# Kernel tuning notes

Measured on AMD Instinct MI355X. Metric: run time of the kernel, lower is better.

Reference implementation:

```python
import jax, jax.numpy as jnp
import numpy as np

D_MODEL = 1024
N_HEADS = 16
D_HEAD = D_MODEL // N_HEADS


def setup_inputs() -> dict:
    key = jax.random.key(0)
    ks = jax.random.split(key, 11)
    B, S = 2, 2048
    scale = 1.0 / np.sqrt(D_MODEL)
    inp = {
        "query": jax.random.normal(ks[0], (B, S, D_MODEL), jnp.float32),
        "key": jax.random.normal(ks[1], (B, S, D_MODEL), jnp.float32),
        "value": jax.random.normal(ks[2], (B, S, D_MODEL), jnp.float32),
        "Wq": jax.random.normal(ks[3], (D_MODEL, D_MODEL), jnp.float32) * scale,
        "bq": jnp.zeros((D_MODEL,), jnp.float32),
        "Wk": jax.random.normal(ks[4], (D_MODEL, D_MODEL), jnp.float32) * scale,
        "bk": jnp.zeros((D_MODEL,), jnp.float32),
        "Wv": jax.random.normal(ks[5], (D_MODEL, D_MODEL), jnp.float32) * scale,
        "bv": jnp.zeros((D_MODEL,), jnp.float32),
        "Wo": jax.random.normal(ks[6], (D_MODEL, D_MODEL), jnp.float32) * scale,
        "bo": jnp.zeros((D_MODEL,), jnp.float32),
    }
    return inp


def _split_heads(x):
    B, S, _ = x.shape
    return x.reshape(B, S, N_HEADS, D_HEAD).transpose(0, 2, 1, 3)  # [B,H,S,Dh]


def reference(query, key, value, Wq, bq, Wk, bk, Wv, bv, Wo, bo):
    q = _split_heads(query @ Wq + bq)
    k = _split_heads(key @ Wk + bk)
    v = _split_heads(value @ Wv + bv)
    # scores [B,H,S,S] -- faithfully materialized as in the original
    scores = jnp.einsum("bhqd,bhkd->bhqk", q, k) / np.sqrt(D_HEAD)
    attn = jax.nn.softmax(scores, axis=-1)
    out = jnp.einsum("bhqk,bhkd->bhqd", attn, v)  # [B,H,S,Dh]
    B, H, S, Dh = out.shape
    out = out.transpose(0, 2, 1, 3).reshape(B, S, H * Dh)
    return out @ Wo + bo
```

## Files before the change

kernel.cpp:

```cpp
#include <hip/hip_runtime.h>
#include <hip/hip_bf16.h>

using bf16 = __hip_bfloat16;
typedef __bf16 bf16x8 __attribute__((ext_vector_type(8)));
typedef __bf16 bf16x2v __attribute__((ext_vector_type(2)));
typedef float f32x4 __attribute__((ext_vector_type(4)));

#define SEQ 2048
#define DM  1024
#define QSCALE 0.18033688011112042f

__device__ __forceinline__ f32x4 mfma16(bf16x8 a, bf16x8 b, f32x4 c) {
  return __builtin_amdgcn_mfma_f32_16x16x32_bf16(a, b, c, 0, 0, 0);
}
__device__ __forceinline__ void gload16(const void* g, void* l) {
  __builtin_amdgcn_global_load_lds(
      (const __attribute__((address_space(1))) unsigned int*)g,
      (__attribute__((address_space(3))) unsigned int*)l, 16, 0, 0);
}
__device__ __forceinline__ unsigned short bfbits(float x) {
  bf16 h = __float2bfloat16(x);
  return *reinterpret_cast<unsigned short*>(&h);
}
__device__ __forceinline__ unsigned pk2(float a, float b) {
#if __has_builtin(__builtin_amdgcn_cvt_pk_bf16_f32)
  bf16x2v r = __builtin_amdgcn_cvt_pk_bf16_f32(a, b);
  return *reinterpret_cast<unsigned*>(&r);
#else
  return (unsigned)bfbits(a) | ((unsigned)bfbits(b) << 16);
#endif
}
__device__ __forceinline__ float fexp2(float x) {
#if __has_builtin(__builtin_amdgcn_exp2f)
  return __builtin_amdgcn_exp2f(x);
#else
  return exp2f(x);
#endif
}

__global__ __launch_bounds__(256) void cast_x(const float* __restrict__ q,
                                              const float* __restrict__ k,
                                              const float* __restrict__ v,
                                              bf16* __restrict__ Lx) {
  const float* src = blockIdx.y == 0 ? q : (blockIdx.y == 1 ? k : v);
  bf16* dst = Lx + (size_t)blockIdx.y * (4096ull * 1024) + (size_t)blockIdx.x * 16384;
#pragma unroll
  for (int i = 0; i < 8; ++i) {
    int u = threadIdx.x + i * 256;
    int k32 = u >> 6, l = u & 63;
    const float* p = src + (size_t)(blockIdx.x * 16 + (l & 15)) * 1024 + k32 * 32 + (l >> 4) * 8;
    float4 a = *(const float4*)p;
    float4 b = *(const float4*)(p + 4);
    alignas(16) unsigned o[4] = {pk2(a.x, a.y), pk2(a.z, a.w), pk2(b.x, b.y), pk2(b.z, b.w)};
    *(uint4*)(dst + (size_t)u * 8) = *(const uint4*)o;
  }
}

__global__ __launch_bounds__(256) void cast_w(const float* __restrict__ Wq,
                                              const float* __restrict__ Wk,
                                              const float* __restrict__ Wv,
                                              const float* __restrict__ Wo,
                                              bf16* __restrict__ Lw,
                                              bf16* __restrict__ Lwo) {
  const int widx = blockIdx.z;
  const float* W = widx == 0 ? Wq : (widx == 1 ? Wk : (widx == 2 ? Wv : Wo));
  bf16* dst = widx < 3 ? (Lw + (size_t)widx * 1048576) : Lwo;
  __shared__ float tf[64][68];
  const int t = threadIdx.x, bx = blockIdx.x, by = blockIdx.y;
#pragma unroll
  for (int i = 0; i < 4; ++i) {
    int u = t + i * 256, r = u >> 4, c4 = u & 15;
    *(float4*)&tf[r][c4 * 4] = *(const float4*)(W + (size_t)(by * 64 + r) * 1024 + bx * 64 + c4 * 4);
  }
  __syncthreads();
#pragma unroll
  for (int i = 0; i < 2; ++i) {
    int u = t + i * 256;
    int sub = u >> 6, l = u & 63;
    int n16l = sub >> 1, k32l = sub & 1;
    int nn = n16l * 16 + (l & 15);
    int kk = k32l * 32 + (l >> 4) * 8;
    alignas(16) unsigned o[4];
#pragma unroll
    for (int p = 0; p < 4; ++p) o[p] = pk2(tf[kk + 2 * p][nn], tf[kk + 2 * p + 1][nn]);
    size_t off = ((((size_t)(bx * 4 + n16l)) * 32 + (by * 2 + k32l)) * 64 + l) * 8;
    *(uint4*)(dst + off) = *(const uint4*)o;
  }
}

__global__ __launch_bounds__(256) void qkv_gemm(const bf16* __restrict__ Lw,
                                                const bf16* __restrict__ Lx,
                                                const float* __restrict__ bq,
                                                const float* __restrict__ bk,
                                                const float* __restrict__ bv,
                                                bf16* __restrict__ Lq,
                                                bf16* __restrict__ Lk,
                                                bf16* __restrict__ Lv) {
  __shared__ alignas(16) bf16 Wl[8192];
  __shared__ alignas(16) bf16 Xl[8192];
  const int t = threadIdx.x, lane = t & 63, w = t >> 6;
  const int m16 = lane & 15, g4 = lane >> 4;
  const int third = blockIdx.y >> 3, mtl = blockIdx.y & 7, nt = blockIdx.x;
  const int wm = w >> 1, wn = w & 1;
  const bf16* Wb = Lw + (size_t)third * 1048576;
  const bf16* Xb = Lx + (size_t)third * (4096ull * 1024);
  f32x4 acc[4][4] = {};

  for (int slab = 0; slab < 16; ++slab) {
#pragma unroll
    for (int ii = 0; ii < 4; ++ii) {
      int s = w * 4 + ii;
      const bf16* gp = Wb + ((((size_t)(mtl * 8 + (s >> 1))) * 32 + slab * 2 + (s & 1)) * 64 + lane) * 8;
      gload16(gp, (void*)&Wl[s * 512]);
    }
#pragma unroll
    for (int ii = 0; ii < 4; ++ii) {
      int s = w * 4 + ii;
      const bf16* gp = Xb + ((((size_t)(nt * 8 + (s >> 1))) * 32 + slab * 2 + (s & 1)) * 64 + lane) * 8;
      gload16(gp, (void*)&Xl[s * 512]);
    }
    __syncthreads();
#pragma unroll
    for (int c = 0; c < 2; ++c) {
      bf16x8 wf[4], xf[4];
#pragma unroll
      for (int i = 0; i < 4; ++i) wf[i] = *(const bf16x8*)&Wl[((wm * 4 + i) * 2 + c) * 512 + lane * 8];
#pragma unroll
      for (int j = 0; j < 4; ++j) xf[j] = *(const bf16x8*)&Xl[((wn * 4 + j) * 2 + c) * 512 + lane * 8];
      if (third < 2) {
#pragma unroll
        for (int i = 0; i < 4; ++i)
#pragma unroll
          for (int j = 0; j < 4; ++j) acc[i][j] = mfma16(wf[i], xf[j], acc[i][j]);
      } else {
#pragma unroll
        for (int i = 0; i < 4; ++i)
#pragma unroll
          for (int j = 0; j < 4; ++j) acc[i][j] = mfma16(xf[i], wf[j], acc[i][j]);
      }
    }
    __syncthreads();
  }

  if (third < 2) {
    bf16* dst = third == 0 ? Lq : Lk;
    const float* bias = third == 0 ? bq : bk;
    const float sc = third == 0 ? QSCALE : 1.0f;
#pragma unroll
    for (int i = 0; i < 4; ++i) {
      int doutb = mtl * 128 + wm * 64 + i * 16 + g4 * 4;
      float4 b4 = *(const float4*)(bias + doutb);
      int hh = doutb >> 6, d32 = (doutb & 63) >> 5;
      int lhi = (doutb & 31) >> 3, half = g4 & 1;
#pragma unroll
      for (int j = 0; j < 4; ++j) {
        int seq = nt * 128 + wn * 64 + j * 16 + m16;
        int bb = seq >> 11, s16w = (seq & 2047) >> 4;
        size_t off = ((((size_t)(bb * 128 + s16w)) * 16 + hh) * 2 + d32) * 512 + (m16 + 16 * lhi) * 8 + half * 4;
        uint2 pv;
        pv.x = pk2((acc[i][j][0] + b4.x) * sc, (acc[i][j][1] + b4.y) * sc);
        pv.y = pk2((acc[i][j][2] + b4.z) * sc, (acc[i][j][3] + b4.w) * sc);
        *(uint2*)(dst + off) = pv;
      }
    }
  } else {
#pragma unroll
    for (int j = 0; j < 4; ++j) {
      int dout = mtl * 128 + wm * 64 + j * 16 + m16;
      float bvv = bv[dout];
      int hh = dout >> 6, dt = (dout & 63) >> 4;
#pragma unroll
      for (int i = 0; i < 4; ++i) {
        int seqb = nt * 128 + wn * 64 + i * 16 + g4 * 4;
        int bb = seqb >> 11, kt = (seqb & 2047) >> 6, ks32 = (seqb & 63) >> 5;
        int lhi = (seqb & 31) >> 3, half = g4 & 1;
        size_t off = (((((size_t)(bb * 32 + kt)) * 16 + hh) * 4 + dt) * 2 + ks32) * 512 + (m16 + 16 * lhi) * 8 + half * 4;
        uint2 pv;
        pv.x = pk2(acc[i][j][0] + bvv, acc[i][j][1] + bvv);
        pv.y = pk2(acc[i][j][2] + bvv, acc[i][j][3] + bvv);
        *(uint2*)(Lv + off) = pv;
      }
    }
  }
}

__global__ __launch_bounds__(256) void flash(const bf16* __restrict__ Lq,
                                             const bf16* __restrict__ Lk,
                                             const bf16* __restrict__ Lv,
                                             bf16* __restrict__ Lab) {
  __shared__ alignas(16) bf16 Kl[2][4096];
  __shared__ alignas(16) bf16 Vl[2][4096];
  __shared__ alignas(16) bf16 Pt[4][32][68];
  const int t = threadIdx.x, lane = t & 63, w = t >> 6;
  const int m16 = lane & 15, g4 = lane >> 4;
  const int bid = blockIdx.x;
  const int qt = bid & 15, h = (bid >> 4) & 15, b = bid >> 8;

  bf16x8 qf[2][2];
#pragma unroll
  for (int q2 = 0; q2 < 2; ++q2)
#pragma unroll
    for (int ks = 0; ks < 2; ++ks)
      qf[q2][ks] = *(const bf16x8*)(Lq +
          ((((size_t)(b * 128 + qt * 8 + w * 2 + q2)) * 16 + h) * 2 + ks) * 512 + lane * 8);

#pragma unroll
  for (int ii = 0; ii < 2; ++ii) {
    int s = w * 2 + ii;
    const bf16* gk = Lk + ((((size_t)(b * 128 + (s >> 1))) * 16 + h) * 2 + (s & 1)) * 512 + lane * 8;
    gload16(gk, (void*)&Kl[0][s * 512]);
    const bf16* gv = Lv + ((((size_t)(b * 32)) * 16 + h) * 8 + s) * 512 + lane * 8;
    gload16(gv, (void*)&Vl[0][s * 512]);
  }

  float lrow[2] = {0.f, 0.f};
  f32x4 oacc[4][2] = {};
  __syncthreads();

  for (int kt = 0; kt < 32; ++kt) {
    const int cur = kt & 1;
    if (kt < 31) {
      int nkt = kt + 1, nb = cur ^ 1;
#pragma unroll
      for (int ii = 0; ii < 2; ++ii) {
        int s = w * 2 + ii;
        const bf16* gk = Lk + ((((size_t)(b * 128 + nkt * 4 + (s >> 1))) * 16 + h) * 2 + (s & 1)) * 512 + lane * 8;
        gload16(gk, (void*)&Kl[nb][s * 512]);
        const bf16* gv = Lv + ((((size_t)(b * 32 + nkt)) * 16 + h) * 8 + s) * 512 + lane * 8;
        gload16(gv, (void*)&Vl[nb][s * 512]);
      }
    }

    f32x4 s[4][2] = {};
#pragma unroll
    for (int ks = 0; ks < 2; ++ks) {
      bf16x8 aK[4];
#pragma unroll
      for (int mt = 0; mt < 4; ++mt) aK[mt] = *(const bf16x8*)&Kl[cur][(mt * 2 + ks) * 512 + lane * 8];
#pragma unroll
      for (int mt = 0; mt < 4; ++mt)
#pragma unroll
        for (int q2 = 0; q2 < 2; ++q2) s[mt][q2] = mfma16(aK[mt], qf[q2][ks], s[mt][q2]);
    }

#pragma unroll
    for (int q2 = 0; q2 < 2; ++q2)
#pragma unroll
      for (int mt = 0; mt < 4; ++mt) {
        float e0 = fexp2(s[mt][q2][0]);
        float e1 = fexp2(s[mt][q2][1]);
        float e2 = fexp2(s[mt][q2][2]);
        float e3 = fexp2(s[mt][q2][3]);
        lrow[q2] += (e0 + e1) + (e2 + e3);
        uint2 pv;
        pv.x = pk2(e0, e1);
        pv.y = pk2(e2, e3);
        *(uint2*)&Pt[w][q2 * 16 + m16][mt * 16 + g4 * 4] = pv;
      }

#pragma unroll
    for (int ks = 0; ks < 2; ++ks) {
      bf16x8 aV[4], bP[2];
#pragma unroll
      for (int dt = 0; dt < 4; ++dt) aV[dt] = *(const bf16x8*)&Vl[cur][(dt * 2 + ks) * 512 + lane * 8];
#pragma unroll
      for (int q2 = 0; q2 < 2; ++q2)
        bP[q2] = *(const bf16x8*)&Pt[w][q2 * 16 + m16][ks * 32 + g4 * 8];
#pragma unroll
      for (int dt = 0; dt < 4; ++dt)
#pragma unroll
        for (int q2 = 0; q2 < 2; ++q2) oacc[dt][q2] = mfma16(aV[dt], bP[q2], oacc[dt][q2]);
    }
    __syncthreads();
  }

#pragma unroll
  for (int q2 = 0; q2 < 2; ++q2) {
    lrow[q2] += __shfl_xor(lrow[q2], 16);
    lrow[q2] += __shfl_xor(lrow[q2], 32);
    float inv = 1.f / lrow[q2];
    int q = b * 2048 + qt * 128 + w * 32 + q2 * 16 + m16;
    int s16g = q >> 4;
#pragma unroll
    for (int dt = 0; dt < 4; ++dt) {
      int dbase = h * 64 + dt * 16 + g4 * 4;
      int k32 = dbase >> 5, lhi = (dbase & 31) >> 3, half = g4 & 1;
      size_t off = ((size_t)s16g * 32 + k32) * 512 + (m16 + 16 * lhi) * 8 + half * 4;
      uint2 pv;
      pv.x = pk2(oacc[dt][q2][0] * inv, oacc[dt][q2][1] * inv);
      pv.y = pk2(oacc[dt][q2][2] * inv, oacc[dt][q2][3] * inv);
      *(uint2*)(Lab + off) = pv;
    }
  }
}

__global__ __launch_bounds__(256) void out_gemm(const bf16* __restrict__ Lab,
                                                const bf16* __restrict__ Lwo,
                                                const float* __restrict__ bo,
                                                float* __restrict__ out) {
  __shared__ alignas(16) bf16 Al[8192];
  __shared__ alignas(16) bf16 Bl[4096];
  const int t = threadIdx.x, lane = t & 63, w = t >> 6;
  const int m16 = lane & 15, g4 = lane >> 4;
  const int nt = blockIdx.x, mt = blockIdx.y;
  const int wm = w >> 1, wn = w & 1;
  f32x4 acc[4][2] = {};

  for (int slab = 0; slab < 16; ++slab) {
#pragma unroll
    for (int ii = 0; ii < 4; ++ii) {
      int s = w * 4 + ii;
      const bf16* gp = Lab + (((size_t)(mt * 8 + (s >> 1))) * 32 + slab * 2 + (s & 1)) * 512 + lane * 8;
      gload16(gp, (void*)&Al[s * 512]);
    }
#pragma unroll
    for (int ii = 0; ii < 2; ++ii) {
      int s = w * 2 + ii;
      const bf16* gp = Lwo + (((size_t)(nt * 4 + (s >> 1))) * 32 + slab * 2 + (s & 1)) * 512 + lane * 8;
      gload16(gp, (void*)&Bl[s * 512]);
    }
    __syncthreads();
#pragma unroll
    for (int c = 0; c < 2; ++c) {
      bf16x8 aA[4], bW[2];
#pragma unroll
      for (int i = 0; i < 4; ++i) aA[i] = *(const bf16x8*)&Al[((wm * 4 + i) * 2 + c) * 512 + lane * 8];
#pragma unroll
      for (int j = 0; j < 2; ++j) bW[j] = *(const bf16x8*)&Bl[((wn * 2 + j) * 2 + c) * 512 + lane * 8];
#pragma unroll
      for (int i = 0; i < 4; ++i)
#pragma unroll
        for (int j = 0; j < 2; ++j) acc[i][j] = mfma16(aA[i], bW[j], acc[i][j]);
    }
    __syncthreads();
  }
#pragma unroll
  for (int j = 0; j < 2; ++j) {
    int n = nt * 64 + wn * 32 + j * 16 + m16;
    float bb = bo[n];
#pragma unroll
    for (int i = 0; i < 4; ++i) {
      int seqb = mt * 128 + wm * 64 + i * 16 + g4 * 4;
#pragma unroll
      for (int r = 0; r < 4; ++r) out[(size_t)(seqb + r) * 1024 + n] = acc[i][j][r] + bb;
    }
  }
}

extern "C" void kernel_launch(void* const* d_in, const int* in_sizes, int n_in,
                              void* d_out, int out_size, void* d_ws, size_t ws_size,
                              hipStream_t stream) {
  const float* query = (const float*)d_in[0];
  const float* key   = (const float*)d_in[1];
  const float* value = (const float*)d_in[2];
  const float* Wq = (const float*)d_in[3];
  const float* bq = (const float*)d_in[4];
  const float* Wk = (const float*)d_in[5];
  const float* bk = (const float*)d_in[6];
  const float* Wv = (const float*)d_in[7];
  const float* bv = (const float*)d_in[8];
  const float* Wo = (const float*)d_in[9];
  const float* bo = (const float*)d_in[10];
  float* out = (float*)d_out;

  bf16* Lw  = (bf16*)d_ws;
  bf16* Lwo = Lw + 3ull * 1048576;
  bf16* Lx  = Lwo + 1048576;
  bf16* Lq  = Lx + 3ull * 4194304;
  bf16* Lk  = Lq + 4194304;
  bf16* Lv  = Lk + 4194304;
  bf16* Lab = Lv + 4194304;

  cast_x<<<dim3(256, 3), 256, 0, stream>>>(query, key, value, Lx);
  cast_w<<<dim3(16, 16, 4), 256, 0, stream>>>(Wq, Wk, Wv, Wo, Lw, Lwo);
  qkv_gemm<<<dim3(32, 24), 256, 0, stream>>>(Lw, Lx, bq, bk, bv, Lq, Lk, Lv);
  flash<<<512, 256, 0, stream>>>(Lq, Lk, Lv, Lab);
  out_gemm<<<dim3(16, 32), 256, 0, stream>>>(Lab, Lwo, bo, out);
}
```

Baseline: 224.6 us.

## Split flash attention KV range across two warp groups with shared-memory combine

The flash kernel now runs 512 threads per block. Two groups of four waves each process half of the key/value sequence with smaller 32-key tiles, and their partial outputs and row sums are merged through shared memory before the normalized result is written. Blocks are also remapped so that consecutive block IDs are spread across heads and batches. The aim is more waves per CU and better latency hiding, at the cost of an extra reduction step and more per-tile synchronisation overhead.

Measured after the change: 215.8 us. 1.04x faster.

```diff
diff --git a/kernel.cpp b/kernel.cpp
--- a/kernel.cpp
+++ b/kernel.cpp
@@ -184,17 +184,23 @@
   }
 }
 
-__global__ __launch_bounds__(256) void flash(const bf16* __restrict__ Lq,
-                                             const bf16* __restrict__ Lk,
-                                             const bf16* __restrict__ Lv,
-                                             bf16* __restrict__ Lab) {
-  __shared__ alignas(16) bf16 Kl[2][4096];
-  __shared__ alignas(16) bf16 Vl[2][4096];
-  __shared__ alignas(16) bf16 Pt[4][32][68];
+__global__ __launch_bounds__(512, 4) void flash(const bf16* __restrict__ Lq,
+                                                const bf16* __restrict__ Lk,
+                                                const bf16* __restrict__ Lv,
+                                                bf16* __restrict__ Lab) {
+  __shared__ alignas(16) unsigned char smem[51200];
+  bf16* const Kb = (bf16*)smem;
+  bf16* const Vb = (bf16*)(smem + 16384);
+  bf16* const Pt = (bf16*)(smem + 32768);
+
   const int t = threadIdx.x, lane = t & 63, w = t >> 6;
   const int m16 = lane & 15, g4 = lane >> 4;
+  const int wg = w & 3, g = w >> 2;
   const int bid = blockIdx.x;
-  const int qt = bid & 15, h = (bid >> 4) & 15, b = bid >> 8;
+  const int logical = ((bid & 7) << 6) | (bid >> 3);
+  const int qt = logical & 15, h = (logical >> 4) & 15, b = logical >> 8;
+
+  bf16* const Ptw = Pt + w * (32 * 36);
 
   bf16x8 qf[2][2];
 #pragma unroll
@@ -202,15 +208,14 @@
 #pragma unroll
     for (int ks = 0; ks < 2; ++ks)
       qf[q2][ks] = *(const bf16x8*)(Lq +
-          ((((size_t)(b * 128 + qt * 8 + w * 2 + q2)) * 16 + h) * 2 + ks) * 512 + lane * 8);
-
-#pragma unroll
-  for (int ii = 0; ii < 2; ++ii) {
-    int s = w * 2 + ii;
-    const bf16* gk = Lk + ((((size_t)(b * 128 + (s >> 1))) * 16 + h) * 2 + (s & 1)) * 512 + lane * 8;
-    gload16(gk, (void*)&Kl[0][s * 512]);
-    const bf16* gv = Lv + ((((size_t)(b * 32)) * 16 + h) * 8 + s) * 512 + lane * 8;
-    gload16(gv, (void*)&Vl[0][s * 512]);
+          ((((size_t)(b * 128 + qt * 8 + wg * 2 + q2)) * 16 + h) * 2 + ks) * 512 + lane * 8);
+
+  const int s16l = wg >> 1, d32 = wg & 1;
+  {
+    const bf16* gk = Lk + ((((size_t)(b * 128 + g * 64 + s16l)) * 16 + h) * 2 + d32) * 512 + lane * 8;
+    gload16(gk, (void*)(Kb + (g * 2 + 0) * 2048 + wg * 512));
+    const bf16* gv = Lv + (((((size_t)(b * 32 + g * 16)) * 16 + h) * 4 + wg) * 2 + 0) * 512 + lane * 8;
+    gload16(gv, (void*)(Vb + (g * 2 + 0) * 2048 + wg * 512));
   }
 
   float lrow[2] = {0.f, 0.f};
@@ -219,26 +224,24 @@
 
   for (int kt = 0; kt < 32; ++kt) {
     const int cur = kt & 1;
+    const bf16* const Kl = Kb + (g * 2 + cur) * 2048;
+    const bf16* const Vl = Vb + (g * 2 + cur) * 2048;
     if (kt < 31) {
-      int nkt = kt + 1, nb = cur ^ 1;
-#pragma unroll
-      for (int ii = 0; ii < 2; ++ii) {
-        int s = w * 2 + ii;
-        const bf16* gk = Lk + ((((size_t)(b * 128 + nkt * 4 + (s >> 1))) * 16 + h) * 2 + (s & 1)) * 512 + lane * 8;
-        gload16(gk, (void*)&Kl[nb][s * 512]);
-        const bf16* gv = Lv + ((((size_t)(b * 32 + nkt)) * 16 + h) * 8 + s) * 512 + lane * 8;
-        gload16(gv, (void*)&Vl[nb][s * 512]);
-      }
-    }
-
-    f32x4 s[4][2] = {};
+      const int nkt = kt + 1, nb = cur ^ 1;
+      const bf16* gk = Lk + ((((size_t)(b * 128 + g * 64 + nkt * 2 + s16l)) * 16 + h) * 2 + d32) * 512 + lane * 8;
+      gload16(gk, (void*)(Kb + (g * 2 + nb) * 2048 + wg * 512));
+      const bf16* gv = Lv + (((((size_t)(b * 32 + g * 16 + (nkt >> 1))) * 16 + h) * 4 + wg) * 2 + (nkt & 1)) * 512 + lane * 8;
+      gload16(gv, (void*)(Vb + (g * 2 + nb) * 2048 + wg * 512));
+    }
+
+    f32x4 s[2][2] = {};
 #pragma unroll
     for (int ks = 0; ks < 2; ++ks) {
-      bf16x8 aK[4];
-#pragma unroll
-      for (int mt = 0; mt < 4; ++mt) aK[mt] = *(const bf16x8*)&Kl[cur][(mt * 2 + ks) * 512 + lane * 8];
-#pragma unroll
-      for (int mt = 0; mt < 4; ++mt)
+      bf16x8 aK[2];
+#pragma unroll
+      for (int mt = 0; mt < 2; ++mt) aK[mt] = *(const bf16x8*)&Kl[(mt * 2 + ks) * 512 + lane * 8];
+#pragma unroll
+      for (int mt = 0; mt < 2; ++mt)
 #pragma unroll
         for (int q2 = 0; q2 < 2; ++q2) s[mt][q2] = mfma16(aK[mt], qf[q2][ks], s[mt][q2]);
     }
@@ -246,7 +249,7 @@
 #pragma unroll
     for (int q2 = 0; q2 < 2; ++q2)
 #pragma unroll
-      for (int mt = 0; mt < 4; ++mt) {
+      for (int mt = 0; mt < 2; ++mt) {
         float e0 = fexp2(s[mt][q2][0]);
         float e1 = fexp2(s[mt][q2][1]);
         float e2 = fexp2(s[mt][q2][2]);
@@ -255,17 +258,20 @@
         uint2 pv;
         pv.x = pk2(e0, e1);
         pv.y = pk2(e2, e3);
-        *(uint2*)&Pt[w][q2 * 16 + m16][mt * 16 + g4 * 4] = pv;
-      }
-
-#pragma unroll
-    for (int ks = 0; ks < 2; ++ks) {
+        *(uint2*)&Ptw[(q2 * 16 + m16) * 36 + mt * 16 + g4 * 4] = pv;
+      }
+
+    {
       bf16x8 aV[4], bP[2];
 #pragma unroll
-      for (int dt = 0; dt < 4; ++dt) aV[dt] = *(const bf16x8*)&Vl[cur][(dt * 2 + ks) * 512 + lane * 8];
-#pragma unroll
-      for (int q2 = 0; q2 < 2; ++q2)
-        bP[q2] = *(const bf16x8*)&Pt[w][q2 * 16 + m16][ks * 32 + g4 * 8];
+      for (int dt = 0; dt < 4; ++dt) aV[dt] = *(const bf16x8*)&Vl[dt * 512 + lane * 8];
+#pragma unroll
+      for (int q2 = 0; q2 < 2; ++q2) {
+        alignas(16) unsigned tmp[4];
+        *(uint2*)&tmp[0] = *(const uint2*)&Ptw[(q2 * 16 + m16) * 36 + g4 * 8];
+        *(uint2*)&tmp[2] = *(const uint2*)&Ptw[(q2 * 16 + m16) * 36 + g4 * 8 + 4];
+        bP[q2] = *(const bf16x8*)tmp;
+      }
 #pragma unroll
       for (int dt = 0; dt < 4; ++dt)
 #pragma unroll
@@ -278,18 +284,39 @@
   for (int q2 = 0; q2 < 2; ++q2) {
     lrow[q2] += __shfl_xor(lrow[q2], 16);
     lrow[q2] += __shfl_xor(lrow[q2], 32);
-    float inv = 1.f / lrow[q2];
-    int q = b * 2048 + qt * 128 + w * 32 + q2 * 16 + m16;
-    int s16g = q >> 4;
-#pragma unroll
-    for (int dt = 0; dt < 4; ++dt) {
-      int dbase = h * 64 + dt * 16 + g4 * 4;
-      int k32 = dbase >> 5, lhi = (dbase & 31) >> 3, half = g4 & 1;
-      size_t off = ((size_t)s16g * 32 + k32) * 512 + (m16 + 16 * lhi) * 8 + half * 4;
-      uint2 pv;
-      pv.x = pk2(oacc[dt][q2][0] * inv, oacc[dt][q2][1] * inv);
-      pv.y = pk2(oacc[dt][q2][2] * inv, oacc[dt][q2][3] * inv);
-      *(uint2*)(Lab + off) = pv;
+  }
+
+  float* const Os = (float*)smem;
+  float* const Ls = (float*)(smem + 32768);
+  if (w >= 4) {
+#pragma unroll
+    for (int dt = 0; dt < 4; ++dt)
+#pragma unroll
+      for (int q2 = 0; q2 < 2; ++q2)
+        *(f32x4*)&Os[(((wg * 4 + dt) * 2 + q2) * 64 + lane) * 4] = oacc[dt][q2];
+    if (g4 == 0) {
+      Ls[(wg * 2 + 0) * 16 + m16] = lrow[0];
+      Ls[(wg * 2 + 1) * 16 + m16] = lrow[1];
+    }
+  }
+  __syncthreads();
+  if (w < 4) {
+#pragma unroll
+    for (int q2 = 0; q2 < 2; ++q2) {
+      float inv = 1.f / (lrow[q2] + Ls[(wg * 2 + q2) * 16 + m16]);
+      int q = b * 2048 + qt * 128 + w * 32 + q2 * 16 + m16;
+      int s16g = q >> 4;
+#pragma unroll
+      for (int dt = 0; dt < 4; ++dt) {
+        f32x4 p = *(const f32x4*)&Os[(((wg * 4 + dt) * 2 + q2) * 64 + lane) * 4];
+        int dbase = h * 64 + dt * 16 + g4 * 4;
+        int k32 = dbase >> 5, lhi = (dbase & 31) >> 3, half = g4 & 1;
+        size_t off = ((size_t)s16g * 32 + k32) * 512 + (m16 + 16 * lhi) * 8 + half * 4;
+        uint2 pv;
+        pv.x = pk2((oacc[dt][q2][0] + p[0]) * inv, (oacc[dt][q2][1] + p[1]) * inv);
+        pv.y = pk2((oacc[dt][q2][2] + p[2]) * inv, (oacc[dt][q2][3] + p[3]) * inv);
+        *(uint2*)(Lab + off) = pv;
+      }
     }
   }
 }
@@ -374,6 +401,6 @@
   cast_x<<<dim3(256, 3), 256, 0, stream>>>(query, key, value, Lx);
   cast_w<<<dim3(16, 16, 4), 256, 0, stream>>>(Wq, Wk, Wv, Wo, Lw, Lwo);
   qkv_gemm<<<dim3(32, 24), 256, 0, stream>>>(Lw, Lx, bq, bk, bv, Lq, Lk, Lv);
-  flash<<<512, 256, 0, stream>>>(Lq, Lk, Lv, Lab);
+  flash<<<512, 512, 0, stream>>>(Lq, Lk, Lv, Lab);
   out_gemm<<<dim3(16, 32), 256, 0, stream>>>(Lab, Lwo, bo, out);
 }
```
